# Performance work log

Hardware: AMD Instinct MI355X
Metric: run time of the kernel (lower is better)

## Reference

```python
import jax, jax.numpy as jnp
import numpy as np

N, B, F, MAXDEG = 100000, 4096, 128, 128
NEI = [25, 10]          # FLAGS.num_neighbors = '25_10'
E1, E2 = 128, 64        # FLAGS.encoder = '128_64'
DEC, C = 256, 50        # FLAGS.decoder, num_classes


def setup_inputs() -> dict:
    key = jax.random.key(0)
    ks = jax.random.split(key, 12)
    return {
        'nodes': jax.random.randint(ks[0], (B,), 0, N),
        'adj_info': jax.random.randint(ks[1], (N, MAXDEG), 0, N),
        'degrees': jax.random.uniform(ks[2], (N,), minval=1.0, maxval=float(MAXDEG)),
        'features': jax.random.normal(ks[3], (N, F), dtype=jnp.float32),
        'W0': jax.random.normal(ks[4], (F, E1), dtype=jnp.float32) / np.sqrt(F),
        'Wm': jax.random.normal(ks[5], (E1, E2), dtype=jnp.float32) / np.sqrt(E1),
        'Ws': jax.random.normal(ks[6], (E1, E2), dtype=jnp.float32) / np.sqrt(E1),
        'W1': jax.random.normal(ks[7], (E2, DEC), dtype=jnp.float32) / np.sqrt(E2),
        'b1': jnp.zeros((DEC,), jnp.float32),
        'W2': jax.random.normal(ks[8], (DEC, C), dtype=jnp.float32) / np.sqrt(DEC),
        'b2': jnp.zeros((C,), jnp.float32),
    }


def _gc(self_v, neigh_v, neigh_d, W, act):
    # GraphSAGE-style degree-normalized mean aggregation + shared linear map
    neigh_mean = jnp.mean(neigh_v / neigh_d, axis=1)   # [n, d_in]
    return act((self_v + neigh_mean) @ W)


def reference(nodes, adj_info, degrees, features, W0, Wm, Ws, W1, b1, W2, b2):
    key = jax.random.key(42)
    k1, k2, k3 = jax.random.split(key, 3)
    # --- uniform neighbor sampling (shared column shuffle, as in TF code) ---
    # hop 1: t = L-1 -> NEI[1] = 10 samples per seed node
    p1 = jax.random.permutation(k1, MAXDEG)[: NEI[1]]
    nb1 = adj_info[nodes][:, p1].reshape(-1)            # [10*B]
    # hop 2: t = 0 -> NEI[0] = 25 samples per hop-1 node
    p2 = jax.random.permutation(k2, MAXDEG)[: NEI[0]]
    nb2 = adj_info[nb1][:, p2].reshape(-1)              # [250*B]

    samples = [nodes, nb1, nb2]
    deg = [degrees[s] for s in samples]
    x = [features[s] for s in samples]                  # [B,F],[10B,F],[250B,F]

    tanh = jnp.tanh
    # layer 0: convolve hops 0 and 1 with shared W0
    h0 = _gc(x[0], x[1].reshape(B, NEI[1], F), deg[1].reshape(B, NEI[1], 1), W0, tanh)
    h1 = _gc(x[1], x[2].reshape(NEI[1] * B, NEI[0], F), deg[2].reshape(NEI[1] * B, NEI[0], 1), W0, tanh)
    # layer 1 (last): mean / std heads, linear activation, hop 0 only
    ident = lambda t: t
    z_mean = _gc(h0, h1.reshape(B, NEI[1], E1), deg[1].reshape(B, NEI[1], 1), Wm, ident)
    z_std = _gc(h0, h1.reshape(B, NEI[1], E1), deg[1].reshape(B, NEI[1], 1), Ws, ident)
    # reparameterized sample (std head = log-std)
    eps = jax.random.normal(k3, z_mean.shape, dtype=z_mean.dtype)
    z = z_mean + eps * jnp.exp(z_std)
    # decoder MLP + softmax class prediction (S = 1 MC sample)
    logits = jax.nn.relu(z @ W1 + b1) @ W2 + b2
    return jax.nn.softmax(logits, axis=-1)
```

## Files before the change

kernel.cpp:

```cpp
#include <hip/hip_runtime.h>
#include <hip/hip_bf16.h>
#include <hip/hip_fp16.h>
#include <stdint.h>
#include <stddef.h>

#define NNODES  100000
#define BATCH   4096
#define FDIM    128
#define MAXDEG  128
#define NEI0    25
#define NEI1    10
#define E1D     128
#define E2D     64
#define DECD    256
#define NCLS    50

#define NH1     (BATCH * NEI1)
#define NROWS   (NH1 + BATCH)

typedef _Float16 half8 __attribute__((ext_vector_type(8)));
typedef float f32x4 __attribute__((ext_vector_type(4)));
typedef float f32x2 __attribute__((ext_vector_type(2)));

__host__ __device__ inline void tf2x32(uint32_t k0, uint32_t k1,
                                       uint32_t x0, uint32_t x1,
                                       uint32_t* o0, uint32_t* o1) {
  uint32_t ks[3] = {k0, k1, k0 ^ k1 ^ 0x1BD11BDAu};
  x0 += ks[0]; x1 += ks[1];
  const int rot[2][4] = {{13, 15, 26, 6}, {17, 29, 16, 24}};
  for (int i = 0; i < 5; ++i) {
    const int* r = rot[i & 1];
    for (int j = 0; j < 4; ++j) {
      x0 += x1;
      x1 = (x1 << r[j]) | (x1 >> (32 - r[j]));
      x1 ^= x0;
    }
    x0 += ks[(i + 1) % 3];
    x1 += ks[(i + 2) % 3] + (uint32_t)(i + 1);
  }
  *o0 = x0; *o1 = x1;
}

__device__ inline float erfinv_xla(float x) {
  float w = -log1pf(-x * x);
  float p;
  if (w < 5.0f) {
    w = w - 2.5f;
    p = 2.81022636e-08f;
    p = 3.43273939e-07f  + p * w;
    p = -3.5233877e-06f  + p * w;
    p = -4.39150654e-06f + p * w;
    p = 0.00021858087f   + p * w;
    p = -0.00125372503f  + p * w;
    p = -0.00417768164f  + p * w;
    p = 0.246640727f     + p * w;
    p = 1.50140941f      + p * w;
  } else {
    w = sqrtf(w) - 3.0f;
    p = -0.000200214257f;
    p = 0.000100950558f  + p * w;
    p = 0.00134934322f   + p * w;
    p = -0.00367342844f  + p * w;
    p = 0.00573950773f   + p * w;
    p = -0.0076224613f   + p * w;
    p = 0.00943887047f   + p * w;
    p = 1.00167406f      + p * w;
    p = 2.83297682f      + p * w;
  }
  return p * x;
}

struct PermArgs { int p1[NEI1]; int p2[NEI0]; };

#define NB1_BLKS   160
#define P2_BLKS    4000
#define SELF_BLKS  2816
#define CAST_FBLKS 12500
#define W0HT_BLKS  8
#define WMST_BLKS  8
#define W1T_BLKS   8
#define W2P_BLKS   8

__global__ __launch_bounds__(256) void prep_kernel(const float* __restrict__ f,
                                                   uint8_t* __restrict__ fh8,
                                                   const float* __restrict__ W0,
                                                   __half* __restrict__ W0ht,
                                                   const float* __restrict__ Wm,
                                                   const float* __restrict__ Wsd,
                                                   __half* __restrict__ Wmst,
                                                   const float* __restrict__ W1,
                                                   __half* __restrict__ W1t,
                                                   const float* __restrict__ W2,
                                                   __half* __restrict__ W2p,
                                                   const int* __restrict__ nodes,
                                                   const int* __restrict__ adj,
                                                   const float* __restrict__ degrees,
                                                   int* __restrict__ nb1,
                                                   float* __restrict__ invd1,
                                                   int* __restrict__ nb2,
                                                   float* __restrict__ invd2,
                                                   __half* __restrict__ selfh,
                                                   PermArgs pa) {
  int bx = blockIdx.x;
  if (bx < NB1_BLKS) {
    int i = bx * 256 + threadIdx.x;
    int b = i / NEI1, j = i - b * NEI1;
    int nn = adj[(size_t)nodes[b] * MAXDEG + pa.p1[j]];
    nb1[i] = nn;
    invd1[i] = 1.0f / degrees[nn];
    return;
  }
  bx -= NB1_BLKS;
  if (bx < P2_BLKS) {
    int i = bx * 256 + threadIdx.x;
    int r = i / NEI0, j = i - r * NEI0;
    int b = r / NEI1, jj = r - b * NEI1;
    int n1 = adj[(size_t)nodes[b] * MAXDEG + pa.p1[jj]];
    int nn = adj[(size_t)n1 * MAXDEG + pa.p2[j]];
    nb2[i] = nn;
    invd2[i] = 1.0f / degrees[nn];
    return;
  }
  bx -= P2_BLKS;
  if (bx < SELF_BLKS) {
    int i = bx * 256 + threadIdx.x;
    int row = i >> 4, cq = (i & 15) * 8;
    int nid;
    if (row < NH1) {
      int b = row / NEI1, jj = row - b * NEI1;
      nid = adj[(size_t)nodes[b] * MAXDEG + pa.p1[jj]];
    } else {
      nid = nodes[row - NH1];
    }
    const float* src = f + (size_t)nid * FDIM + cq;
    float4 a = *(const float4*)src;
    float4 b4 = *(const float4*)(src + 4);
    uint4 ov; uint32_t* op = (uint32_t*)&ov;
    op[0] = __builtin_bit_cast(uint32_t, __floats2half2_rn(a.x, a.y));
    op[1] = __builtin_bit_cast(uint32_t, __floats2half2_rn(a.z, a.w));
    op[2] = __builtin_bit_cast(uint32_t, __floats2half2_rn(b4.x, b4.y));
    op[3] = __builtin_bit_cast(uint32_t, __floats2half2_rn(b4.z, b4.w));
    *(uint4*)(selfh + (size_t)row * FDIM + cq) = ov;
    return;
  }
  bx -= SELF_BLKS;
  if (bx < CAST_FBLKS) {
    int i = bx * 256 + threadIdx.x;
    float4 v = ((const float4*)f)[i];
    int p = 0;
    p = __builtin_amdgcn_cvt_pk_fp8_f32(v.x, v.y, p, false);
    p = __builtin_amdgcn_cvt_pk_fp8_f32(v.z, v.w, p, true);
    ((int*)fh8)[i] = p;
    return;
  }
  bx -= CAST_FBLKS;
  if (bx < W0HT_BLKS) {
    int i = bx * 256 + threadIdx.x;
    int n = i >> 4, kb = (i & 15) * 8;
    uint4 ov; uint32_t* op = (uint32_t*)&ov;
#pragma unroll
    for (int q = 0; q < 4; ++q) {
      __half2 h = __floats2half2_rn(W0[(size_t)(kb + 2 * q) * E1D + n],
                                    W0[(size_t)(kb + 2 * q + 1) * E1D + n]);
      op[q] = __builtin_bit_cast(uint32_t, h);
    }
    *(uint4*)(W0ht + (size_t)n * FDIM + kb) = ov;
    return;
  }
  bx -= W0HT_BLKS;
  if (bx < WMST_BLKS) {
    int i = bx * 256 + threadIdx.x;
    int n = i >> 4, kb = (i & 15) * 8;
    const float* src = (n < E2D) ? (Wm + n) : (Wsd + (n - E2D));
    uint4 ov; uint32_t* op = (uint32_t*)&ov;
#pragma unroll
    for (int q = 0; q < 4; ++q) {
      __half2 h = __floats2half2_rn(src[(size_t)(kb + 2 * q) * E2D],
                                    src[(size_t)(kb + 2 * q + 1) * E2D]);
      op[q] = __builtin_bit_cast(uint32_t, h);
    }
    *(uint4*)(Wmst + (size_t)n * E1D + kb) = ov;
    return;
  }
  bx -= WMST_BLKS;
  if (bx < W1T_BLKS) {
    int i = bx * 256 + threadIdx.x;
    int n = i >> 3, kb = (i & 7) * 8;
    uint4 ov; uint32_t* op = (uint32_t*)&ov;
#pragma unroll
    for (int q = 0; q < 4; ++q) {
      __half2 h = __floats2half2_rn(W1[(size_t)(kb + 2 * q) * DECD + n],
                                    W1[(size_t)(kb + 2 * q + 1) * DECD + n]);
      op[q] = __builtin_bit_cast(uint32_t, h);
    }
    *(uint4*)(W1t + (size_t)n * E2D + kb) = ov;
    return;
  }
  bx -= W1T_BLKS;
  {
    int i = bx * 256 + threadIdx.x;
    int c = i >> 5, kb = (i & 31) * 8;
    uint4 ov; uint32_t* op = (uint32_t*)&ov;
#pragma unroll
    for (int q = 0; q < 4; ++q) {
      float a = (c < NCLS) ? W2[(size_t)(kb + 2 * q) * NCLS + c] : 0.0f;
      float b = (c < NCLS) ? W2[(size_t)(kb + 2 * q + 1) * NCLS + c] : 0.0f;
      __half2 h = __floats2half2_rn(a, b);
      op[q] = __builtin_bit_cast(uint32_t, h);
    }
    *(uint4*)(W2p + (size_t)c * DECD + kb) = ov;
  }
}

#define CONSV8(vv, idv) do { \
    float id_ = (idv); \
    f32x2 c0_ = __builtin_amdgcn_cvt_pk_f32_fp8((int)(vv).x, false); \
    f32x2 c1_ = __builtin_amdgcn_cvt_pk_f32_fp8((int)(vv).x, true); \
    f32x2 c2_ = __builtin_amdgcn_cvt_pk_f32_fp8((int)(vv).y, false); \
    f32x2 c3_ = __builtin_amdgcn_cvt_pk_f32_fp8((int)(vv).y, true); \
    acc0 += c0_[0] * id_; acc1 += c0_[1] * id_; \
    acc2 += c1_[0] * id_; acc3 += c1_[1] * id_; \
    acc4 += c2_[0] * id_; acc5 += c2_[1] * id_; \
    acc6 += c3_[0] * id_; acc7 += c3_[1] * id_; \
  } while (0)

#define H8(x) __builtin_bit_cast(half8, x)

__global__ __launch_bounds__(256) void sage0_kernel(const int* __restrict__ nodes,
                                                    const int* __restrict__ nb1,
                                                    const float* __restrict__ invd1,
                                                    const int* __restrict__ nb2,
                                                    const float* __restrict__ invd2,
                                                    const uint8_t* __restrict__ fh8,
                                                    const __half* __restrict__ selfh,
                                                    const __half* __restrict__ W0ht,
                                                    __half* __restrict__ hh) {
  const int t = threadIdx.x;
  const int blk = blockIdx.x;
  const bool typeA = blk < (NH1 / 16);
  const int row_base = typeA ? blk * 16 : NH1 + (blk - NH1 / 16) * 16;
  __shared__ int    nn_lds[16][NEI0];
  __shared__ float  id_lds[16][NEI0];
  __shared__ __half agg_h[16][FDIM];

  if (typeA) {
    for (int i = t; i < 16 * NEI0; i += 256) {
      int r = i / NEI0, j = i - r * NEI0;
      nn_lds[r][j] = nb2[row_base * NEI0 + i];
      id_lds[r][j] = invd2[row_base * NEI0 + i];
    }
  } else {
    const int sb = row_base - NH1;
    if (t < 16 * NEI1) {
      int r = t / NEI1, j = t - r * NEI1;
      nn_lds[r][j] = nb1[sb * NEI1 + t];
      id_lds[r][j] = invd1[sb * NEI1 + t];
    }
  }
  __syncthreads();

  const int l = t & 63, w = t >> 6;
  const int r  = w * 4 + (l >> 4);
  const int c0 = (l & 15) * 8;
  const uint8_t* fr8 = fh8 + c0;
  const int*   nn_r = nn_lds[r];
  const float* id_r = id_lds[r];

  float acc0 = 0, acc1 = 0, acc2 = 0, acc3 = 0, acc4 = 0, acc5 = 0, acc6 = 0, acc7 = 0;
  uint4 gs = *(const uint4*)(selfh + (size_t)(row_base + r) * FDIM + c0);
  if (typeA) {
    uint2 g0  = *(const uint2*)(fr8 + (size_t)nn_r[0]  * FDIM);
    uint2 g1  = *(const uint2*)(fr8 + (size_t)nn_r[1]  * FDIM);
    uint2 g2  = *(const uint2*)(fr8 + (size_t)nn_r[2]  * FDIM);
    uint2 g3  = *(const uint2*)(fr8 + (size_t)nn_r[3]  * FDIM);
    uint2 g4  = *(const uint2*)(fr8 + (size_t)nn_r[4]  * FDIM);
    uint2 g5  = *(const uint2*)(fr8 + (size_t)nn_r[5]  * FDIM);
    uint2 g6  = *(const uint2*)(fr8 + (size_t)nn_r[6]  * FDIM);
    uint2 g7  = *(const uint2*)(fr8 + (size_t)nn_r[7]  * FDIM);
    uint2 g8  = *(const uint2*)(fr8 + (size_t)nn_r[8]  * FDIM);
    uint2 g9  = *(const uint2*)(fr8 + (size_t)nn_r[9]  * FDIM);
    uint2 g10 = *(const uint2*)(fr8 + (size_t)nn_r[10] * FDIM);
    uint2 g11 = *(const uint2*)(fr8 + (size_t)nn_r[11] * FDIM);
    uint2 g12 = *(const uint2*)(fr8 + (size_t)nn_r[12] * FDIM);
    uint2 g13 = *(const uint2*)(fr8 + (size_t)nn_r[13] * FDIM);
    uint2 g14 = *(const uint2*)(fr8 + (size_t)nn_r[14] * FDIM);
    uint2 g15 = *(const uint2*)(fr8 + (size_t)nn_r[15] * FDIM);
    uint2 g16 = *(const uint2*)(fr8 + (size_t)nn_r[16] * FDIM);
    uint2 g17 = *(const uint2*)(fr8 + (size_t)nn_r[17] * FDIM);
    uint2 g18 = *(const uint2*)(fr8 + (size_t)nn_r[18] * FDIM);
    uint2 g19 = *(const uint2*)(fr8 + (size_t)nn_r[19] * FDIM);
    uint2 g20 = *(const uint2*)(fr8 + (size_t)nn_r[20] * FDIM);
    uint2 g21 = *(const uint2*)(fr8 + (size_t)nn_r[21] * FDIM);
    uint2 g22 = *(const uint2*)(fr8 + (size_t)nn_r[22] * FDIM);
    uint2 g23 = *(const uint2*)(fr8 + (size_t)nn_r[23] * FDIM);
    uint2 g24 = *(const uint2*)(fr8 + (size_t)nn_r[24] * FDIM);
    __builtin_amdgcn_sched_barrier(0);
    CONSV8(g0,  id_r[0]);  CONSV8(g1,  id_r[1]);  CONSV8(g2,  id_r[2]);
    CONSV8(g3,  id_r[3]);  CONSV8(g4,  id_r[4]);  CONSV8(g5,  id_r[5]);
    CONSV8(g6,  id_r[6]);  CONSV8(g7,  id_r[7]);  CONSV8(g8,  id_r[8]);
    CONSV8(g9,  id_r[9]);  CONSV8(g10, id_r[10]); CONSV8(g11, id_r[11]);
    CONSV8(g12, id_r[12]); CONSV8(g13, id_r[13]); CONSV8(g14, id_r[14]);
    CONSV8(g15, id_r[15]); CONSV8(g16, id_r[16]); CONSV8(g17, id_r[17]);
    CONSV8(g18, id_r[18]); CONSV8(g19, id_r[19]); CONSV8(g20, id_r[20]);
    CONSV8(g21, id_r[21]); CONSV8(g22, id_r[22]); CONSV8(g23, id_r[23]);
    CONSV8(g24, id_r[24]);
  } else {
    uint2 g0 = *(const uint2*)(fr8 + (size_t)nn_r[0] * FDIM);
    uint2 g1 = *(const uint2*)(fr8 + (size_t)nn_r[1] * FDIM);
    uint2 g2 = *(const uint2*)(fr8 + (size_t)nn_r[2] * FDIM);
    uint2 g3 = *(const uint2*)(fr8 + (size_t)nn_r[3] * FDIM);
    uint2 g4 = *(const uint2*)(fr8 + (size_t)nn_r[4] * FDIM);
    uint2 g5 = *(const uint2*)(fr8 + (size_t)nn_r[5] * FDIM);
    uint2 g6 = *(const uint2*)(fr8 + (size_t)nn_r[6] * FDIM);
    uint2 g7 = *(const uint2*)(fr8 + (size_t)nn_r[7] * FDIM);
    uint2 g8 = *(const uint2*)(fr8 + (size_t)nn_r[8] * FDIM);
    uint2 g9 = *(const uint2*)(fr8 + (size_t)nn_r[9] * FDIM);
    __builtin_amdgcn_sched_barrier(0);
    CONSV8(g0, id_r[0]); CONSV8(g1, id_r[1]); CONSV8(g2, id_r[2]);
    CONSV8(g3, id_r[3]); CONSV8(g4, id_r[4]); CONSV8(g5, id_r[5]);
    CONSV8(g6, id_r[6]); CONSV8(g7, id_r[7]); CONSV8(g8, id_r[8]);
    CONSV8(g9, id_r[9]);
  }
  {
    const float sc = typeA ? (1.0f / NEI0) : (1.0f / NEI1);
    const __half2* sp = (const __half2*)&gs;
    float2 s0 = __half22float2(sp[0]);
    float2 s1 = __half22float2(sp[1]);
    float2 s2 = __half22float2(sp[2]);
    float2 s3 = __half22float2(sp[3]);
    uint4 ov; uint32_t* op = (uint32_t*)&ov;
    __half2 o0 = __floats2half2_rn(s0.x + acc0 * sc, s0.y + acc1 * sc);
    __half2 o1 = __floats2half2_rn(s1.x + acc2 * sc, s1.y + acc3 * sc);
    __half2 o2 = __floats2half2_rn(s2.x + acc4 * sc, s2.y + acc5 * sc);
    __half2 o3 = __floats2half2_rn(s3.x + acc6 * sc, s3.y + acc7 * sc);
    op[0] = __builtin_bit_cast(uint32_t, o0);
    op[1] = __builtin_bit_cast(uint32_t, o1);
    op[2] = __builtin_bit_cast(uint32_t, o2);
    op[3] = __builtin_bit_cast(uint32_t, o3);
    char* wb = (char*)agg_h + r * 256 + ((c0 * 2) ^ ((r & 7) << 4));
    *(uint4*)wb = ov;
  }
  __syncthreads();

  {
    const int lr = l & 15, kq = l >> 4;
    const __half* wt0 = W0ht + (size_t)(w * 32 + lr) * FDIM + kq * 8;
    const __half* wt1 = wt0 + 16 * FDIM;
    uint4 b00 = *(const uint4*)(wt0 + 0);
    uint4 b01 = *(const uint4*)(wt0 + 32);
    uint4 b02 = *(const uint4*)(wt0 + 64);
    uint4 b03 = *(const uint4*)(wt0 + 96);
    uint4 b10 = *(const uint4*)(wt1 + 0);
    uint4 b11 = *(const uint4*)(wt1 + 32);
    uint4 b12 = *(const uint4*)(wt1 + 64);
    uint4 b13 = *(const uint4*)(wt1 + 96);
    const char* ab = (const char*)agg_h + lr * 256;
    const int sw = (lr & 7) << 4;
    uint4 a0 = *(const uint4*)(ab + ((0 * 64 + kq * 16) ^ sw));
    uint4 a1 = *(const uint4*)(ab + ((1 * 64 + kq * 16) ^ sw));
    uint4 a2 = *(const uint4*)(ab + ((2 * 64 + kq * 16) ^ sw));
    uint4 a3 = *(const uint4*)(ab + ((3 * 64 + kq * 16) ^ sw));
    f32x4 cA = {0, 0, 0, 0}, cB = {0, 0, 0, 0};
    cA = __builtin_amdgcn_mfma_f32_16x16x32_f16(H8(a0), H8(b00), cA, 0, 0, 0);
    cB = __builtin_amdgcn_mfma_f32_16x16x32_f16(H8(a0), H8(b10), cB, 0, 0, 0);
    cA = __builtin_amdgcn_mfma_f32_16x16x32_f16(H8(a1), H8(b01), cA, 0, 0, 0);
    cB = __builtin_amdgcn_mfma_f32_16x16x32_f16(H8(a1), H8(b11), cB, 0, 0, 0);
    cA = __builtin_amdgcn_mfma_f32_16x16x32_f16(H8(a2), H8(b02), cA, 0, 0, 0);
    cB = __builtin_amdgcn_mfma_f32_16x16x32_f16(H8(a2), H8(b12), cB, 0, 0, 0);
    cA = __builtin_amdgcn_mfma_f32_16x16x32_f16(H8(a3), H8(b03), cA, 0, 0, 0);
    cB = __builtin_amdgcn_mfma_f32_16x16x32_f16(H8(a3), H8(b13), cB, 0, 0, 0);
    const int orow = row_base + (l >> 4) * 4;
    const int colA = w * 32 + lr, colB = colA + 16;
#pragma unroll
    for (int m = 0; m < 4; ++m) {
      hh[(size_t)(orow + m) * E1D + colA] = __float2half(tanhf(cA[m]));
      hh[(size_t)(orow + m) * E1D + colB] = __float2half(tanhf(cB[m]));
    }
  }
}

__global__ __launch_bounds__(256) void encdec_kernel(const float* __restrict__ invd1,
                                                     const __half* __restrict__ hh,
                                                     const __half* __restrict__ Wmst,
                                                     const __half* __restrict__ W1t,
                                                     const float* __restrict__ b1,
                                                     const __half* __restrict__ W2p,
                                                     const float* __restrict__ b2,
                                                     float* __restrict__ out,
                                                     uint32_t k3a, uint32_t k3b) {
  const int t = threadIdx.x;
  const int s0 = blockIdx.x * 16;
  __shared__ float  id_lds[16][NEI1];
  __shared__ __half agg_h[16][FDIM];
  __shared__ float  P[16 * 132];
  __shared__ __half zA[16 * E2D];
  __shared__ float  hidF[16][260];
  __shared__ float  lgF[16][68];

  if (t < 16 * NEI1) {
    int r = t / NEI1, j = t - r * NEI1;
    id_lds[r][j] = invd1[s0 * NEI1 + t];
  }
  __syncthreads();

  const int l = t & 63, w = t >> 6;
  const int lr = l & 15, kq = l >> 4;

  {
    const int r  = w * 4 + (l >> 4);
    const int c0 = (l & 15) * 8;
    float acc0 = 0, acc1 = 0, acc2 = 0, acc3 = 0, acc4 = 0, acc5 = 0, acc6 = 0, acc7 = 0;
    const float* id_r = id_lds[r];
#pragma unroll
    for (int j = 0; j < NEI1; ++j) {
      uint4 vv = *(const uint4*)(hh + (size_t)((s0 + r) * NEI1 + j) * E1D + c0);
      const __half2* hp_ = (const __half2*)&vv;
      float id_ = id_r[j];
      float2 f0_ = __half22float2(hp_[0]);
      float2 f1_ = __half22float2(hp_[1]);
      float2 f2_ = __half22float2(hp_[2]);
      float2 f3_ = __half22float2(hp_[3]);
      acc0 += f0_.x * id_; acc1 += f0_.y * id_;
      acc2 += f1_.x * id_; acc3 += f1_.y * id_;
      acc4 += f2_.x * id_; acc5 += f2_.y * id_;
      acc6 += f3_.x * id_; acc7 += f3_.y * id_;
    }
    uint4 sv = *(const uint4*)(hh + (size_t)(NH1 + s0 + r) * E1D + c0);
    const float sc = 1.0f / NEI1;
    const __half2* sp = (const __half2*)&sv;
    float2 s0f = __half22float2(sp[0]);
    float2 s1f = __half22float2(sp[1]);
    float2 s2f = __half22float2(sp[2]);
    float2 s3f = __half22float2(sp[3]);
    uint4 ov; uint32_t* op = (uint32_t*)&ov;
    __half2 o0 = __floats2half2_rn(s0f.x + acc0 * sc, s0f.y + acc1 * sc);
    __half2 o1 = __floats2half2_rn(s1f.x + acc2 * sc, s1f.y + acc3 * sc);
    __half2 o2 = __floats2half2_rn(s2f.x + acc4 * sc, s2f.y + acc5 * sc);
    __half2 o3 = __floats2half2_rn(s3f.x + acc6 * sc, s3f.y + acc7 * sc);
    op[0] = __builtin_bit_cast(uint32_t, o0);
    op[1] = __builtin_bit_cast(uint32_t, o1);
    op[2] = __builtin_bit_cast(uint32_t, o2);
    op[3] = __builtin_bit_cast(uint32_t, o3);
    char* wb = (char*)agg_h + r * 256 + ((c0 * 2) ^ ((r & 7) << 4));
    *(uint4*)wb = ov;
  }
  __syncthreads();

  {
    const __half* wt0 = Wmst + (size_t)(w * 32 + lr) * FDIM + kq * 8;
    const __half* wt1 = wt0 + 16 * FDIM;
    uint4 b00 = *(const uint4*)(wt0 + 0);
    uint4 b01 = *(const uint4*)(wt0 + 32);
    uint4 b02 = *(const uint4*)(wt0 + 64);
    uint4 b03 = *(const uint4*)(wt0 + 96);
    uint4 b10 = *(const uint4*)(wt1 + 0);
    uint4 b11 = *(const uint4*)(wt1 + 32);
    uint4 b12 = *(const uint4*)(wt1 + 64);
    uint4 b13 = *(const uint4*)(wt1 + 96);
    const char* ab = (const char*)agg_h + lr * 256;
    const int sw = (lr & 7) << 4;
    uint4 a0 = *(const uint4*)(ab + ((0 * 64 + kq * 16) ^ sw));
    uint4 a1 = *(const uint4*)(ab + ((1 * 64 + kq * 16) ^ sw));
    uint4 a2 = *(const uint4*)(ab + ((2 * 64 + kq * 16) ^ sw));
    uint4 a3 = *(const uint4*)(ab + ((3 * 64 + kq * 16) ^ sw));
    f32x4 cA = {0, 0, 0, 0}, cB = {0, 0, 0, 0};
    cA = __builtin_amdgcn_mfma_f32_16x16x32_f16(H8(a0), H8(b00), cA, 0, 0, 0);
    cB = __builtin_amdgcn_mfma_f32_16x16x32_f16(H8(a0), H8(b10), cB, 0, 0, 0);
    cA = __builtin_amdgcn_mfma_f32_16x16x32_f16(H8(a1), H8(b01), cA, 0, 0, 0);
    cB = __builtin_amdgcn_mfma_f32_16x16x32_f16(H8(a1), H8(b11), cB, 0, 0, 0);
    cA = __builtin_amdgcn_mfma_f32_16x16x32_f16(H8(a2), H8(b02), cA, 0, 0, 0);
    cB = __builtin_amdgcn_mfma_f32_16x16x32_f16(H8(a2), H8(b12), cB, 0, 0, 0);
    cA = __builtin_amdgcn_mfma_f32_16x16x32_f16(H8(a3), H8(b03), cA, 0, 0, 0);
    cB = __builtin_amdgcn_mfma_f32_16x16x32_f16(H8(a3), H8(b13), cB, 0, 0, 0);
    const int orow = kq * 4;
    const int colA = w * 32 + lr, colB = colA + 16;
#pragma unroll
    for (int m = 0; m < 4; ++m) {
      P[(orow + m) * 132 + colA] = cA[m];
      P[(orow + m) * 132 + colB] = cB[m];
    }
  }
  __syncthreads();

  {
    const int r2 = t >> 4;
    const int cb = (t & 15) * 4;
    uint32_t ph[2];
#pragma unroll
    for (int h = 0; h < 2; ++h) {
      float zv[2];
#pragma unroll
      for (int g = 0; g < 2; ++g) {
        int c = cb + 2 * h + g;
        uint32_t ctr = (uint32_t)((s0 + r2) * E2D + c);
        uint32_t y0, y1;
        tf2x32(k3a, k3b, 0u, ctr, &y0, &y1);
        uint32_t bits = y0 ^ y1;
        uint32_t fb = (bits >> 9) | 0x3F800000u;
        float fl = __uint_as_float(fb) - 1.0f;
        const float lo = -0.99999994f;
        float u = fmaxf(lo, fl * 2.0f + lo);
        float eps = 1.4142135381698608f * erfinv_xla(u);
        zv[g] = P[r2 * 132 + c] + eps * expf(P[r2 * 132 + c + E2D]);
      }
      ph[h] = __builtin_bit_cast(uint32_t, __floats2half2_rn(zv[0], zv[1]));
    }
    char* p = (char*)zA + ((r2 * 128 + cb * 2) ^ ((r2 & 7) << 4));
    *(uint2*)p = make_uint2(ph[0], ph[1]);
  }
  __syncthreads();

  {
    const char* zb = (const char*)zA + lr * 128;
    const int sw = (lr & 7) << 4;
    uint4 a0 = *(const uint4*)(zb + ((0 + kq * 16) ^ sw));
    uint4 a1 = *(const uint4*)(zb + ((64 + kq * 16) ^ sw));
#define G1STEP(CT) { \
    int n = w * 64 + (CT) * 16 + lr; \
    uint4 b0 = *(const uint4*)(W1t + (size_t)n * E2D + kq * 8); \
    uint4 b1v = *(const uint4*)(W1t + (size_t)n * E2D + 32 + kq * 8); \
    f32x4 cc = {0, 0, 0, 0}; \
    cc = __builtin_amdgcn_mfma_f32_16x16x32_f16(H8(a0), H8(b0), cc, 0, 0, 0); \
    cc = __builtin_amdgcn_mfma_f32_16x16x32_f16(H8(a1), H8(b1v), cc, 0, 0, 0); \
    float bv = b1[n]; \
    hidF[kq * 4 + 0][n] = fmaxf(cc[0] + bv, 0.0f); \
    hidF[kq * 4 + 1][n] = fmaxf(cc[1] + bv, 0.0f); \
    hidF[kq * 4 + 2][n] = fmaxf(cc[2] + bv, 0.0f); \
    hidF[kq * 4 + 3][n] = fmaxf(cc[3] + bv, 0.0f); }
    G1STEP(0) G1STEP(1) G1STEP(2) G1STEP(3)
#undef G1STEP
  }
  __syncthreads();

  {
    f32x4 d = {0, 0, 0, 0};
    const __half* w2b = W2p + (size_t)(w * 16 + lr) * DECD + kq * 8;
#pragma unroll
    for (int ks = 0; ks < 8; ++ks) {
      float4 fA = *(const float4*)&hidF[lr][ks * 32 + kq * 8];
      float4 fB = *(const float4*)&hidF[lr][ks * 32 + kq * 8 + 4];
      uint4 ap;
      uint32_t* app = (uint32_t*)&ap;
      app[0] = __builtin_bit_cast(uint32_t, __floats2half2_rn(fA.x, fA.y));
      app[1] = __builtin_bit_cast(uint32_t, __floats2half2_rn(fA.z, fA.w));
      app[2] = __builtin_bit_cast(uint32_t, __floats2half2_rn(fB.x, fB.y));
      app[3] = __builtin_bit_cast(uint32_t, __floats2half2_rn(fB.z, fB.w));
      uint4 bfr = *(const uint4*)(w2b + ks * 32);
      d = __builtin_amdgcn_mfma_f32_16x16x32_f16(H8(ap), H8(bfr), d, 0, 0, 0);
    }
    int col = w * 16 + lr;
    float bb = (col < NCLS) ? b2[col] : 0.0f;
#pragma unroll
    for (int m = 0; m < 4; ++m) lgF[kq * 4 + m][col] = d[m] + bb;
  }
  __syncthreads();

  {
#pragma unroll
    for (int rr = 0; rr < 4; ++rr) {
      int row = w * 4 + rr;
      float v = (l < NCLS) ? lgF[row][l] : -3.0e38f;
      float m = v;
#pragma unroll
      for (int off = 32; off; off >>= 1) m = fmaxf(m, __shfl_xor(m, off));
      float e = (l < NCLS) ? expf(v - m) : 0.0f;
      float s = e;
#pragma unroll
      for (int off = 32; off; off >>= 1) s += __shfl_xor(s, off);
      if (l < NCLS) out[(size_t)(s0 + row) * NCLS + l] = e / s;
    }
  }
}

static void host_permutation(uint32_t ka, uint32_t kb, int count, int* out_idx) {
  uint32_t sa, sb;
  tf2x32(ka, kb, 0u, 1u, &sa, &sb);
  uint32_t keys[MAXDEG];
  int vals[MAXDEG];
  for (int i = 0; i < MAXDEG; ++i) {
    uint32_t y0, y1;
    tf2x32(sa, sb, 0u, (uint32_t)i, &y0, &y1);
    keys[i] = y0 ^ y1;
    vals[i] = i;
  }
  for (int i = 1; i < MAXDEG; ++i) {
    uint32_t kk = keys[i]; int vv = vals[i]; int j = i - 1;
    while (j >= 0 && keys[j] > kk) { keys[j+1] = keys[j]; vals[j+1] = vals[j]; --j; }
    keys[j+1] = kk; vals[j+1] = vv;
  }
  for (int i = 0; i < count; ++i) out_idx[i] = vals[i];
}

extern "C" void kernel_launch(void* const* d_in, const int* in_sizes, int n_in,
                              void* d_out, int out_size, void* d_ws, size_t ws_size,
                              hipStream_t stream) {
  const int*   nodes    = (const int*)  d_in[0];
  const int*   adj      = (const int*)  d_in[1];
  const float* degrees  = (const float*)d_in[2];
  const float* features = (const float*)d_in[3];
  const float* W0       = (const float*)d_in[4];
  const float* Wm       = (const float*)d_in[5];
  const float* Wsd      = (const float*)d_in[6];
  const float* W1       = (const float*)d_in[7];
  const float* b1       = (const float*)d_in[8];
  const float* W2       = (const float*)d_in[9];
  const float* b2       = (const float*)d_in[10];
  float* out = (float*)d_out;

  uint32_t k1a, k1b, k2a, k2b, k3a, k3b;
  tf2x32(0u, 42u, 0u, 0u, &k1a, &k1b);
  tf2x32(0u, 42u, 0u, 1u, &k2a, &k2b);
  tf2x32(0u, 42u, 0u, 2u, &k3a, &k3b);

  PermArgs pa;
  host_permutation(k1a, k1b, NEI1, pa.p1);
  host_permutation(k2a, k2b, NEI0, pa.p2);

  char* ws = (char*)d_ws;
  int*     nb1   = (int*)    (ws + 0);
  float*   invd1 = (float*)  (ws + 163840);
  int*     nb2   = (int*)    (ws + 327680);
  float*   invd2 = (float*)  (ws + 4423680);
  __half*  hh    = (__half*) (ws + 8519680);
  uint8_t* fh8   = (uint8_t*)(ws + 20054016);
  __half*  selfh = (__half*) (ws + 32854016);
  __half*  W0ht  = (__half*) (ws + 44388352);
  __half*  Wmst  = (__half*) (ws + 44421120);
  __half*  W1t   = (__half*) (ws + 44453888);
  __half*  W2p   = (__half*) (ws + 44486656);

  prep_kernel<<<NB1_BLKS + P2_BLKS + SELF_BLKS + CAST_FBLKS +
                W0HT_BLKS + WMST_BLKS + W1T_BLKS + W2P_BLKS, 256, 0, stream>>>(
      features, fh8, W0, W0ht, Wm, Wsd, Wmst, W1, W1t, W2, W2p,
      nodes, adj, degrees, nb1, invd1, nb2, invd2, selfh, pa);
  sage0_kernel<<<NROWS / 16, 256, 0, stream>>>(
      nodes, nb1, invd1, nb2, invd2, fh8, selfh, W0ht, hh);
  encdec_kernel<<<BATCH / 16, 256, 0, stream>>>(
      invd1, hh, Wmst, W1t, b1, W2p, b2, out, k3a, k3b);
}
```

Measured before the change: 68.01 us.

## Quantize gathered features to 4-bit FP4-like codes and reuse half self rows for hop-1

Replaces the FP8 copy of the full feature table with a 4-bit E2M1-style encoding (thresholded magnitude plus sign), halving the bytes gathered for the 25-neighbour hop-2 aggregation. Decoding uses a byte-permute lookup into FP8 constants. Seed-row aggregation now reads hop-1 neighbour rows from the already materialized half-precision selfh buffer instead of gathering FP8 rows by index. The trade is a much coarser quantization of features, which could break accuracy tolerance.

```diff
diff --git a/kernel.cpp b/kernel.cpp
--- a/kernel.cpp
+++ b/kernel.cpp
@@ -75,14 +75,14 @@
 #define NB1_BLKS   160
 #define P2_BLKS    4000
 #define SELF_BLKS  2816
-#define CAST_FBLKS 12500
+#define CAST_FBLKS 6250
 #define W0HT_BLKS  8
 #define WMST_BLKS  8
 #define W1T_BLKS   8
 #define W2P_BLKS   8
 
 __global__ __launch_bounds__(256) void prep_kernel(const float* __restrict__ f,
-                                                   uint8_t* __restrict__ fh8,
+                                                   uint8_t* __restrict__ fh4,
                                                    const float* __restrict__ W0,
                                                    __half* __restrict__ W0ht,
                                                    const float* __restrict__ Wm,
@@ -146,11 +146,22 @@
   bx -= SELF_BLKS;
   if (bx < CAST_FBLKS) {
     int i = bx * 256 + threadIdx.x;
-    float4 v = ((const float4*)f)[i];
-    int p = 0;
-    p = __builtin_amdgcn_cvt_pk_fp8_f32(v.x, v.y, p, false);
-    p = __builtin_amdgcn_cvt_pk_fp8_f32(v.z, v.w, p, true);
-    ((int*)fh8)[i] = p;
+    float4 va = ((const float4*)f)[2 * i];
+    float4 vb = ((const float4*)f)[2 * i + 1];
+    float xs[8] = {va.x, va.y, va.z, va.w, vb.x, vb.y, vb.z, vb.w};
+    uint32_t wd = 0;
+#pragma unroll
+    for (int k = 0; k < 8; ++k) {
+      float x = xs[k];
+      float a = fabsf(x);
+      uint32_t n = (uint32_t)(a >= 0.25f) + (uint32_t)(a >= 0.75f) +
+                   (uint32_t)(a >= 1.25f) + (uint32_t)(a >= 1.75f) +
+                   (uint32_t)(a >= 2.5f)  + (uint32_t)(a >= 3.5f) +
+                   (uint32_t)(a >= 5.0f);
+      uint32_t nib = n ? (n | ((__float_as_uint(x) >> 28) & 8u)) : 0u;
+      wd |= nib << (4 * k);
+    }
+    ((uint32_t*)fh4)[i] = wd;
     return;
   }
   bx -= CAST_FBLKS;
@@ -212,26 +223,44 @@
   }
 }
 
-#define CONSV8(vv, idv) do { \
+#define CONSVH(vv, idv) do { \
+    const __half2* hp_ = (const __half2*)&(vv); \
     float id_ = (idv); \
-    f32x2 c0_ = __builtin_amdgcn_cvt_pk_f32_fp8((int)(vv).x, false); \
-    f32x2 c1_ = __builtin_amdgcn_cvt_pk_f32_fp8((int)(vv).x, true); \
-    f32x2 c2_ = __builtin_amdgcn_cvt_pk_f32_fp8((int)(vv).y, false); \
-    f32x2 c3_ = __builtin_amdgcn_cvt_pk_f32_fp8((int)(vv).y, true); \
-    acc0 += c0_[0] * id_; acc1 += c0_[1] * id_; \
-    acc2 += c1_[0] * id_; acc3 += c1_[1] * id_; \
-    acc4 += c2_[0] * id_; acc5 += c2_[1] * id_; \
-    acc6 += c3_[0] * id_; acc7 += c3_[1] * id_; \
+    float2 f0_ = __half22float2(hp_[0]); \
+    float2 f1_ = __half22float2(hp_[1]); \
+    float2 f2_ = __half22float2(hp_[2]); \
+    float2 f3_ = __half22float2(hp_[3]); \
+    acc0 += f0_.x * id_; acc1 += f0_.y * id_; \
+    acc2 += f1_.x * id_; acc3 += f1_.y * id_; \
+    acc4 += f2_.x * id_; acc5 += f2_.y * id_; \
+    acc6 += f3_.x * id_; acc7 += f3_.y * id_; \
   } while (0)
 
+#define CONSV4(vv, idv) do { \
+    float id_ = (idv); \
+    uint32_t ei_ = (vv) & 0x07070707u; \
+    uint32_t oi_ = ((vv) >> 4) & 0x07070707u; \
+    uint32_t es_ = ((vv) << 4) & 0x80808080u; \
+    uint32_t os_ = (vv) & 0x80808080u; \
+    uint32_t fe_ = __builtin_amdgcn_perm((uint32_t)lutHi, (uint32_t)lutLo, ei_) | es_; \
+    uint32_t fo_ = __builtin_amdgcn_perm((uint32_t)lutHi, (uint32_t)lutLo, oi_) | os_; \
+    f32x2 c0_ = __builtin_amdgcn_cvt_pk_f32_fp8((int)fe_, false); \
+    f32x2 c1_ = __builtin_amdgcn_cvt_pk_f32_fp8((int)fe_, true); \
+    f32x2 c2_ = __builtin_amdgcn_cvt_pk_f32_fp8((int)fo_, false); \
+    f32x2 c3_ = __builtin_amdgcn_cvt_pk_f32_fp8((int)fo_, true); \
+    acc0 += c0_[0] * id_; acc2 += c0_[1] * id_; \
+    acc4 += c1_[0] * id_; acc6 += c1_[1] * id_; \
+    acc1 += c2_[0] * id_; acc3 += c2_[1] * id_; \
+    acc5 += c3_[0] * id_; acc7 += c3_[1] * id_; \
+  } while (0)
+
 #define H8(x) __builtin_bit_cast(half8, x)
 
 __global__ __launch_bounds__(256) void sage0_kernel(const int* __restrict__ nodes,
-                                                    const int* __restrict__ nb1,
                                                     const float* __restrict__ invd1,
                                                     const int* __restrict__ nb2,
                                                     const float* __restrict__ invd2,
-                                                    const uint8_t* __restrict__ fh8,
+                                                    const uint8_t* __restrict__ fh4,
                                                     const __half* __restrict__ selfh,
                                                     const __half* __restrict__ W0ht,
                                                     __half* __restrict__ hh) {
@@ -253,7 +282,6 @@
     const int sb = row_base - NH1;
     if (t < 16 * NEI1) {
       int r = t / NEI1, j = t - r * NEI1;
-      nn_lds[r][j] = nb1[sb * NEI1 + t];
       id_lds[r][j] = invd1[sb * NEI1 + t];
     }
   }
@@ -262,64 +290,73 @@
   const int l = t & 63, w = t >> 6;
   const int r  = w * 4 + (l >> 4);
   const int c0 = (l & 15) * 8;
-  const uint8_t* fr8 = fh8 + c0;
-  const int*   nn_r = nn_lds[r];
   const float* id_r = id_lds[r];
 
   float acc0 = 0, acc1 = 0, acc2 = 0, acc3 = 0, acc4 = 0, acc5 = 0, acc6 = 0, acc7 = 0;
   uint4 gs = *(const uint4*)(selfh + (size_t)(row_base + r) * FDIM + c0);
+
+  int lutLo = 0, lutHi = 0;
+  lutLo = __builtin_amdgcn_cvt_pk_fp8_f32(0.0f, 0.5f, lutLo, false);
+  lutLo = __builtin_amdgcn_cvt_pk_fp8_f32(1.0f, 1.5f, lutLo, true);
+  lutHi = __builtin_amdgcn_cvt_pk_fp8_f32(2.0f, 3.0f, lutHi, false);
+  lutHi = __builtin_amdgcn_cvt_pk_fp8_f32(4.0f, 6.0f, lutHi, true);
+
   if (typeA) {
-    uint2 g0  = *(const uint2*)(fr8 + (size_t)nn_r[0]  * FDIM);
-    uint2 g1  = *(const uint2*)(fr8 + (size_t)nn_r[1]  * FDIM);
-    uint2 g2  = *(const uint2*)(fr8 + (size_t)nn_r[2]  * FDIM);
-    uint2 g3  = *(const uint2*)(fr8 + (size_t)nn_r[3]  * FDIM);
-    uint2 g4  = *(const uint2*)(fr8 + (size_t)nn_r[4]  * FDIM);
-    uint2 g5  = *(const uint2*)(fr8 + (size_t)nn_r[5]  * FDIM);
-    uint2 g6  = *(const uint2*)(fr8 + (size_t)nn_r[6]  * FDIM);
-    uint2 g7  = *(const uint2*)(fr8 + (size_t)nn_r[7]  * FDIM);
-    uint2 g8  = *(const uint2*)(fr8 + (size_t)nn_r[8]  * FDIM);
-    uint2 g9  = *(const uint2*)(fr8 + (size_t)nn_r[9]  * FDIM);
-    uint2 g10 = *(const uint2*)(fr8 + (size_t)nn_r[10] * FDIM);
-    uint2 g11 = *(const uint2*)(fr8 + (size_t)nn_r[11] * FDIM);
-    uint2 g12 = *(const uint2*)(fr8 + (size_t)nn_r[12] * FDIM);
-    uint2 g13 = *(const uint2*)(fr8 + (size_t)nn_r[13] * FDIM);
-    uint2 g14 = *(const uint2*)(fr8 + (size_t)nn_r[14] * FDIM);
-    uint2 g15 = *(const uint2*)(fr8 + (size_t)nn_r[15] * FDIM);
-    uint2 g16 = *(const uint2*)(fr8 + (size_t)nn_r[16] * FDIM);
-    uint2 g17 = *(const uint2*)(fr8 + (size_t)nn_r[17] * FDIM);
-    uint2 g18 = *(const uint2*)(fr8 + (size_t)nn_r[18] * FDIM);
-    uint2 g19 = *(const uint2*)(fr8 + (size_t)nn_r[19] * FDIM);
-    uint2 g20 = *(const uint2*)(fr8 + (size_t)nn_r[20] * FDIM);
-    uint2 g21 = *(const uint2*)(fr8 + (size_t)nn_r[21] * FDIM);
-    uint2 g22 = *(const uint2*)(fr8 + (size_t)nn_r[22] * FDIM);
-    uint2 g23 = *(const uint2*)(fr8 + (size_t)nn_r[23] * FDIM);
-    uint2 g24 = *(const uint2*)(fr8 + (size_t)nn_r[24] * FDIM);
+    const int* nn_r = nn_lds[r];
+    const uint8_t* fr4 = fh4 + (c0 >> 1);
+    uint32_t g0  = *(const uint32_t*)(fr4 + (size_t)nn_r[0]  * 64);
+    uint32_t g1  = *(const uint32_t*)(fr4 + (size_t)nn_r[1]  * 64);
+    uint32_t g2  = *(const uint32_t*)(fr4 + (size_t)nn_r[2]  * 64);
+    uint32_t g3  = *(const uint32_t*)(fr4 + (size_t)nn_r[3]  * 64);
+    uint32_t g4  = *(const uint32_t*)(fr4 + (size_t)nn_r[4]  * 64);
+    uint32_t g5  = *(const uint32_t*)(fr4 + (size_t)nn_r[5]  * 64);
+    uint32_t g6  = *(const uint32_t*)(fr4 + (size_t)nn_r[6]  * 64);
+    uint32_t g7  = *(const uint32_t*)(fr4 + (size_t)nn_r[7]  * 64);
+    uint32_t g8  = *(const uint32_t*)(fr4 + (size_t)nn_r[8]  * 64);
+    uint32_t g9  = *(const uint32_t*)(fr4 + (size_t)nn_r[9]  * 64);
+    uint32_t g10 = *(const uint32_t*)(fr4 + (size_t)nn_r[10] * 64);
+    uint32_t g11 = *(const uint32_t*)(fr4 + (size_t)nn_r[11] * 64);
+    uint32_t g12 = *(const uint32_t*)(fr4 + (size_t)nn_r[12] * 64);
+    uint32_t g13 = *(const uint32_t*)(fr4 + (size_t)nn_r[13] * 64);
+    uint32_t g14 = *(const uint32_t*)(fr4 + (size_t)nn_r[14] * 64);
+    uint32_t g15 = *(const uint32_t*)(fr4 + (size_t)nn_r[15] * 64);
+    uint32_t g16 = *(const uint32_t*)(fr4 + (size_t)nn_r[16] * 64);
+    uint32_t g17 = *(const uint32_t*)(fr4 + (size_t)nn_r[17] * 64);
+    uint32_t g18 = *(const uint32_t*)(fr4 + (size_t)nn_r[18] * 64);
+    uint32_t g19 = *(const uint32_t*)(fr4 + (size_t)nn_r[19] * 64);
+    uint32_t g20 = *(const uint32_t*)(fr4 + (size_t)nn_r[20] * 64);
+    uint32_t g21 = *(const uint32_t*)(fr4 + (size_t)nn_r[21] * 64);
+    uint32_t g22 = *(const uint32_t*)(fr4 + (size_t)nn_r[22] * 64);
+    uint32_t g23 = *(const uint32_t*)(fr4 + (size_t)nn_r[23] * 64);
+    uint32_t g24 = *(const uint32_t*)(fr4 + (size_t)nn_r[24] * 64);
     __builtin_amdgcn_sched_barrier(0);
-    CONSV8(g0,  id_r[0]);  CONSV8(g1,  id_r[1]);  CONSV8(g2,  id_r[2]);
-    CONSV8(g3,  id_r[3]);  CONSV8(g4,  id_r[4]);  CONSV8(g5,  id_r[5]);
-    CONSV8(g6,  id_r[6]);  CONSV8(g7,  id_r[7]);  CONSV8(g8,  id_r[8]);
-    CONSV8(g9,  id_r[9]);  CONSV8(g10, id_r[10]); CONSV8(g11, id_r[11]);
-    CONSV8(g12, id_r[12]); CONSV8(g13, id_r[13]); CONSV8(g14, id_r[14]);
-    CONSV8(g15, id_r[15]); CONSV8(g16, id_r[16]); CONSV8(g17, id_r[17]);
-    CONSV8(g18, id_r[18]); CONSV8(g19, id_r[19]); CONSV8(g20, id_r[20]);
-    CONSV8(g21, id_r[21]); CONSV8(g22, id_r[22]); CONSV8(g23, id_r[23]);
-    CONSV8(g24, id_r[24]);
+    CONSV4(g0,  id_r[0]);  CONSV4(g1,  id_r[1]);  CONSV4(g2,  id_r[2]);
+    CONSV4(g3,  id_r[3]);  CONSV4(g4,  id_r[4]);  CONSV4(g5,  id_r[5]);
+    CONSV4(g6,  id_r[6]);  CONSV4(g7,  id_r[7]);  CONSV4(g8,  id_r[8]);
+    CONSV4(g9,  id_r[9]);  CONSV4(g10, id_r[10]); CONSV4(g11, id_r[11]);
+    CONSV4(g12, id_r[12]); CONSV4(g13, id_r[13]); CONSV4(g14, id_r[14]);
+    CONSV4(g15, id_r[15]); CONSV4(g16, id_r[16]); CONSV4(g17, id_r[17]);
+    CONSV4(g18, id_r[18]); CONSV4(g19, id_r[19]); CONSV4(g20, id_r[20]);
+    CONSV4(g21, id_r[21]); CONSV4(g22, id_r[22]); CONSV4(g23, id_r[23]);
+    CONSV4(g24, id_r[24]);
   } else {
-    uint2 g0 = *(const uint2*)(fr8 + (size_t)nn_r[0] * FDIM);
-    uint2 g1 = *(const uint2*)(fr8 + (size_t)nn_r[1] * FDIM);
-    uint2 g2 = *(const uint2*)(fr8 + (size_t)nn_r[2] * FDIM);
-    uint2 g3 = *(const uint2*)(fr8 + (size_t)nn_r[3] * FDIM);
-    uint2 g4 = *(const uint2*)(fr8 + (size_t)nn_r[4] * FDIM);
-    uint2 g5 = *(const uint2*)(fr8 + (size_t)nn_r[5] * FDIM);
-    uint2 g6 = *(const uint2*)(fr8 + (size_t)nn_r[6] * FDIM);
-    uint2 g7 = *(const uint2*)(fr8 + (size_t)nn_r[7] * FDIM);
-    uint2 g8 = *(const uint2*)(fr8 + (size_t)nn_r[8] * FDIM);
-    uint2 g9 = *(const uint2*)(fr8 + (size_t)nn_r[9] * FDIM);
+    const int sb = row_base - NH1;
+    const __half* nbase = selfh + (size_t)(sb + r) * NEI1 * FDIM + c0;
+    uint4 g0 = *(const uint4*)(nbase + 0 * FDIM);
+    uint4 g1 = *(const uint4*)(nbase + 1 * FDIM);
+    uint4 g2 = *(const uint4*)(nbase + 2 * FDIM);
+    uint4 g3 = *(const uint4*)(nbase + 3 * FDIM);
+    uint4 g4 = *(const uint4*)(nbase + 4 * FDIM);
+    uint4 g5 = *(const uint4*)(nbase + 5 * FDIM);
+    uint4 g6 = *(const uint4*)(nbase + 6 * FDIM);
+    uint4 g7 = *(const uint4*)(nbase + 7 * FDIM);
+    uint4 g8 = *(const uint4*)(nbase + 8 * FDIM);
+    uint4 g9 = *(const uint4*)(nbase + 9 * FDIM);
     __builtin_amdgcn_sched_barrier(0);
-    CONSV8(g0, id_r[0]); CONSV8(g1, id_r[1]); CONSV8(g2, id_r[2]);
-    CONSV8(g3, id_r[3]); CONSV8(g4, id_r[4]); CONSV8(g5, id_r[5]);
-    CONSV8(g6, id_r[6]); CONSV8(g7, id_r[7]); CONSV8(g8, id_r[8]);
-    CONSV8(g9, id_r[9]);
+    CONSVH(g0, id_r[0]); CONSVH(g1, id_r[1]); CONSVH(g2, id_r[2]);
+    CONSVH(g3, id_r[3]); CONSVH(g4, id_r[4]); CONSVH(g5, id_r[5]);
+    CONSVH(g6, id_r[6]); CONSVH(g7, id_r[7]); CONSVH(g8, id_r[8]);
+    CONSVH(g9, id_r[9]);
   }
   {
     const float sc = typeA ? (1.0f / NEI0) : (1.0f / NEI1);
@@ -414,16 +451,7 @@
 #pragma unroll
     for (int j = 0; j < NEI1; ++j) {
       uint4 vv = *(const uint4*)(hh + (size_t)((s0 + r) * NEI1 + j) * E1D + c0);
-      const __half2* hp_ = (const __half2*)&vv;
-      float id_ = id_r[j];
-      float2 f0_ = __half22float2(hp_[0]);
-      float2 f1_ = __half22float2(hp_[1]);
-      float2 f2_ = __half22float2(hp_[2]);
-      float2 f3_ = __half22float2(hp_[3]);
-      acc0 += f0_.x * id_; acc1 += f0_.y * id_;
-      acc2 += f1_.x * id_; acc3 += f1_.y * id_;
-      acc4 += f2_.x * id_; acc5 += f2_.y * id_;
-      acc6 += f3_.x * id_; acc7 += f3_.y * id_;
+      CONSVH(vv, id_r[j]);
     }
     uint4 sv = *(const uint4*)(hh + (size_t)(NH1 + s0 + r) * E1D + c0);
     const float sc = 1.0f / NEI1;
@@ -622,19 +650,19 @@
   int*     nb2   = (int*)    (ws + 327680);
   float*   invd2 = (float*)  (ws + 4423680);
   __half*  hh    = (__half*) (ws + 8519680);
-  uint8_t* fh8   = (uint8_t*)(ws + 20054016);
-  __half*  selfh = (__half*) (ws + 32854016);
-  __half*  W0ht  = (__half*) (ws + 44388352);
-  __half*  Wmst  = (__half*) (ws + 44421120);
-  __half*  W1t   = (__half*) (ws + 44453888);
-  __half*  W2p   = (__half*) (ws + 44486656);
+  __half*  selfh = (__half*) (ws + 20054016);
+  uint8_t* fh4   = (uint8_t*)(ws + 31588352);
+  __half*  W0ht  = (__half*) (ws + 37988352);
+  __half*  Wmst  = (__half*) (ws + 38021120);
+  __half*  W1t   = (__half*) (ws + 38053888);
+  __half*  W2p   = (__half*) (ws + 38086656);
 
   prep_kernel<<<NB1_BLKS + P2_BLKS + SELF_BLKS + CAST_FBLKS +
                 W0HT_BLKS + WMST_BLKS + W1T_BLKS + W2P_BLKS, 256, 0, stream>>>(
-      features, fh8, W0, W0ht, Wm, Wsd, Wmst, W1, W1t, W2, W2p,
+      features, fh4, W0, W0ht, Wm, Wsd, Wmst, W1, W1t, W2, W2p,
       nodes, adj, degrees, nb1, invd1, nb2, invd2, selfh, pa);
   sage0_kernel<<<NROWS / 16, 256, 0, stream>>>(
-      nodes, nb1, invd1, nb2, invd2, fh8, selfh, W0ht, hh);
+      nodes, invd1, nb2, invd2, fh4, selfh, W0ht, hh);
   encdec_kernel<<<BATCH / 16, 256, 0, stream>>>(
       invd1, hh, Wmst, W1t, b1, W2p, b2, out, k3a, k3b);
 }
```

Result: no change. 66.72 us (-1.9%).
